# Performance work log

Hardware: AMD Instinct MI355X
Metric: run time of the kernel (lower is better)

## Reference

```python
import jax, jax.numpy as jnp
import numpy as np

H = 8        # heads
DH = 64      # dim_head
K = 16       # num_neighbors
EMB = 512    # emb_dim
INNER = H * DH
AINNER = 4 * DH  # per-head attn_mlp hidden width
POSH = 64


def setup_inputs() -> dict:
    key = jax.random.key(0)
    ks = jax.random.split(key, 20)
    bs, n = 2, 1024
    rn = lambda k, s, sc=1.0: jax.random.normal(k, s, jnp.float32) * sc
    return {
        "query": rn(ks[0], (bs, n, EMB)),
        "key_in": rn(ks[1], (bs, n, EMB)),
        "value": rn(ks[2], (bs, n, EMB)),
        "canonical": rn(ks[3], (bs, n, 3)),
        "w_q": rn(ks[4], (EMB, INNER), EMB ** -0.5),
        "w_k": rn(ks[5], (EMB, INNER), EMB ** -0.5),
        "w_v": rn(ks[6], (EMB, INNER), EMB ** -0.5),
        "w_out": rn(ks[7], (INNER, EMB), INNER ** -0.5),
        "b_out": rn(ks[8], (EMB,), 0.02),
        "pos_w1": rn(ks[9], (3, POSH), 3 ** -0.5),
        "pos_b1": rn(ks[10], (POSH,), 0.02),
        "pos_w2": rn(ks[11], (POSH, INNER), POSH ** -0.5),
        "pos_b2": rn(ks[12], (INNER,), 0.02),
        "aw1": rn(ks[13], (H, AINNER, DH), DH ** -0.5),   # grouped conv1 weight per head: (out=4*DH, in=DH)
        "ab1": rn(ks[14], (H, AINNER), 0.02),
        "aw2": rn(ks[15], (H, DH, AINNER), AINNER ** -0.5),  # grouped conv2: (out=DH, in=4*DH)
        "ab2": rn(ks[16], (H, DH), 0.02),
    }


def reference(query, key_in, value, canonical, w_q, w_k, w_v, w_out, b_out,
              pos_w1, pos_b1, pos_w2, pos_b2, aw1, ab1, aw2, ab2):
    bs, n, _ = query.shape
    # projections, then b n (h d) -> b h n d
    to_heads = lambda t: t.reshape(bs, n, H, DH).transpose(0, 2, 1, 3)
    q = to_heads(query @ w_q)
    k = to_heads(key_in @ w_k)
    v = to_heads(value @ w_v)

    # KNN on canonical coords: (b,n,n) squared distances, k smallest (includes self)
    d2 = jnp.sum((canonical[:, :, None, :] - canonical[:, None, :, :]) ** 2, axis=-1)
    _, nbr = jax.lax.top_k(-d2, K)                       # (b,n,K)
    idx = (nbr + (jnp.arange(bs) * n)[:, None, None]).reshape(-1)  # flat rows into bs*n

    # relative position embedding
    pos_nn = canonical.reshape(bs * n, 3)[idx].reshape(bs, n, K, 3)
    rel = pos_nn - canonical[:, :, None, :]
    rpe = jax.nn.relu(rel @ pos_w1 + pos_b1) @ pos_w2 + pos_b2        # (b,n,K,inner)
    rpe = rpe.reshape(bs, n, K, H, DH).transpose(0, 3, 1, 2, 4)       # (b,h,i,j,d)

    # faithful replication of the original view(bs*n,-1)[idx] gathers on (b,h,n,d) tensors
    gather = lambda t: t.reshape(bs * n, -1)[idx].reshape(bs, H, n, K, DH)
    qg, kg, vg = gather(q), gather(k), gather(v)
    vg = vg + rpe
    x = (qg - kg) + rpe                                  # (b,h,i,j,d)

    # grouped 1x1 conv attn_mlp == per-head MLP over d
    hdn = jax.nn.relu(jnp.einsum('bhijd,hed->bhije', x, aw1) + ab1[None, :, None, None, :])
    sim = jnp.einsum('bhije,hde->bhijd', hdn, aw2) + ab2[None, :, None, None, :]

    attn = jax.nn.softmax(sim, axis=3)                   # softmax over neighbors j
    norm = jnp.sqrt(jnp.sum(attn * attn, axis=2, keepdims=True))  # F.normalize over i
    attn = attn / jnp.maximum(norm, 1e-12)

    agg = jnp.einsum('bhijd,bhijd->bhid', attn, vg)      # (b,h,i,d)
    agg = agg.transpose(0, 2, 1, 3).reshape(bs, n, INNER)
    return agg @ w_out + b_out
```

## Files before the change

### kernel.cpp

```cpp
#include <hip/hip_runtime.h>


#define BS 2
#define NPT 1024
#define HH 8
#define DH 64
#define KNN 16
#define EMB 512
#define INNER 512
#define AINNER 256
#define POSH 64

typedef unsigned short u16;
typedef unsigned int u32;
typedef __attribute__((ext_vector_type(8))) short bf16x8;
typedef __attribute__((ext_vector_type(4))) float f32x4;

__device__ __forceinline__ float bf2f(u16 b) { union { u32 u; float f; } v; v.u = ((u32)b) << 16; return v.f; }
__device__ __forceinline__ u16 f2bf_rne(float f) {
    u32 x = __float_as_uint(f);
    u32 r = x + 0x7fffu + ((x >> 16) & 1u);
    return (u16)(r >> 16);
}
__device__ __forceinline__ void split2(float f, u16& hi, u16& lo) {
    u32 bits = __float_as_uint(f);
    hi = (u16)(bits >> 16);
    float resid = f - __uint_as_float(bits & 0xffff0000u);
    lo = (u16)(__float_as_uint(resid) >> 16);
}
__device__ __forceinline__ void split4(float4 f, ushort4& h, ushort4& l) {
    split2(f.x, h.x, l.x); split2(f.y, h.y, l.y);
    split2(f.z, h.z, l.z); split2(f.w, h.w, l.w);
}

__global__ __launch_bounds__(256) void k_pre(const float* __restrict__ aw1,
                                             const float* __restrict__ aw2,
                                             const float* __restrict__ pw2,
                                             u16* __restrict__ w1hi, u16* __restrict__ w2hi,
                                             u16* __restrict__ rw2hi)
{
    int idx = blockIdx.x * 256 + threadIdx.x;
    if (idx < 131072) {
        w1hi[idx] = f2bf_rne(aw1[idx]);
    } else if (idx < 262144) {
        int k2 = idx - 131072;
        w2hi[k2] = f2bf_rne(aw2[k2]);
    } else {
        int k2 = idx - 262144;
        int p = k2 & 63; int hd = k2 >> 6;
        int h = hd >> 6; int d = hd & 63;
        rw2hi[k2] = f2bf_rne(pw2[(size_t)p * INNER + h * DH + d]);
    }
}

__global__ __launch_bounds__(256) void k_split_T(const float* __restrict__ wq,
                                                 const float* __restrict__ wk,
                                                 const float* __restrict__ wv,
                                                 const float* __restrict__ wout,
                                                 u16* __restrict__ o0h, u16* __restrict__ o0l,
                                                 u16* __restrict__ o1h, u16* __restrict__ o1l,
                                                 u16* __restrict__ o2h, u16* __restrict__ o2l,
                                                 u16* __restrict__ o3h, u16* __restrict__ o3l)
{
    __shared__ float S[64][65];
    const int t = threadIdx.x;
    const int e0 = blockIdx.x * 64, c0 = blockIdx.y * 64;
    const float* src; u16* dh; u16* dl;
    switch (blockIdx.z) {
        case 0:  src = wq;   dh = o0h; dl = o0l; break;
        case 1:  src = wk;   dh = o1h; dl = o1l; break;
        case 2:  src = wv;   dh = o2h; dl = o2l; break;
        default: src = wout; dh = o3h; dl = o3l; break;
    }
    #pragma unroll
    for (int s = 0; s < 16; ++s) {
        int v = s * 256 + t; int r = v >> 6, c = v & 63;
        S[r][c] = src[(size_t)(e0 + r) * 512 + c0 + c];
    }
    __syncthreads();
    #pragma unroll
    for (int s = 0; s < 16; ++s) {
        int v = s * 256 + t; int c = v >> 6, e = v & 63;
        u16 hi, lo; split2(S[e][c], hi, lo);
        size_t off = (size_t)(c0 + c) * 512 + e0 + e;
        dh[off] = hi; dl[off] = lo;
    }
}

__global__ __launch_bounds__(256) void k_projM(const float* __restrict__ qf,
                                               const float* __restrict__ kf,
                                               const float* __restrict__ vf,
                                               const u16* __restrict__ wqh, const u16* __restrict__ wql,
                                               const u16* __restrict__ wkh, const u16* __restrict__ wkl,
                                               const u16* __restrict__ wvh, const u16* __restrict__ wvl,
                                               float* __restrict__ Dws, float* __restrict__ Vws)
{
    __shared__ u16 S[12][64 * 40];
    const int t = threadIdx.x, l = t & 63, w = t >> 6;
    const int lm = l & 15, lg = (l >> 4) * 8;
    const int g0 = blockIdx.x * 64, c0 = blockIdx.y * 64;
    const int sr = t >> 2, sc = (t & 3) * 8;

    f32x4 accD[4] = {{0,0,0,0},{0,0,0,0},{0,0,0,0},{0,0,0,0}};
    f32x4 accV[4] = {{0,0,0,0},{0,0,0,0},{0,0,0,0},{0,0,0,0}};

    const float* asrc0 = qf; const float* asrc1 = kf; const float* asrc2 = vf;

    for (int ks = 0; ks < 16; ++ks) {
        const int k0 = ks * 32;
        if (ks) __syncthreads();
        #pragma unroll
        for (int m = 0; m < 3; ++m) {
            const float* sp = (m == 0 ? asrc0 : (m == 1 ? asrc1 : asrc2))
                              + (size_t)(g0 + sr) * 512 + k0 + sc;
            float4 f0 = *(const float4*)sp;
            float4 f1 = *(const float4*)(sp + 4);
            if (m == 1) {
                f0.x = -f0.x; f0.y = -f0.y; f0.z = -f0.z; f0.w = -f0.w;
                f1.x = -f1.x; f1.y = -f1.y; f1.z = -f1.z; f1.w = -f1.w;
            }
            ushort4 h0, l0, h1, l1;
            split4(f0, h0, l0); split4(f1, h1, l1);
            *(ushort4*)&S[2*m  ][sr * 40 + sc]     = h0;
            *(ushort4*)&S[2*m  ][sr * 40 + sc + 4] = h1;
            *(ushort4*)&S[2*m+1][sr * 40 + sc]     = l0;
            *(ushort4*)&S[2*m+1][sr * 40 + sc + 4] = l1;
        }
        #define STG(p, base) \
            *(uint4*)&S[p][sr * 40 + sc] = *(const uint4*)&(base)[(size_t)(c0 + sr) * 512 + k0 + sc];
        STG(6, wqh) STG(7, wql) STG(8, wkh) STG(9, wkl) STG(10, wvh) STG(11, wvl)
        #undef STG
        __syncthreads();

        const int ao = (w * 16 + lm) * 40 + lg;
        bf16x8 aqh = *(const bf16x8*)&S[0][ao];
        bf16x8 aql = *(const bf16x8*)&S[1][ao];
        bf16x8 akh = *(const bf16x8*)&S[2][ao];
        bf16x8 akl = *(const bf16x8*)&S[3][ao];
        bf16x8 avh = *(const bf16x8*)&S[4][ao];
        bf16x8 avl = *(const bf16x8*)&S[5][ao];
        #pragma unroll
        for (int ct = 0; ct < 4; ++ct) {
            const int bo = (ct * 16 + lm) * 40 + lg;
            bf16x8 bqh = *(const bf16x8*)&S[6][bo];
            bf16x8 bql = *(const bf16x8*)&S[7][bo];
            bf16x8 bkh = *(const bf16x8*)&S[8][bo];
            bf16x8 bkl = *(const bf16x8*)&S[9][bo];
            bf16x8 bvh = *(const bf16x8*)&S[10][bo];
            bf16x8 bvl = *(const bf16x8*)&S[11][bo];
            accD[ct] = __builtin_amdgcn_mfma_f32_16x16x32_bf16(aqh, bqh, accD[ct], 0, 0, 0);
            accD[ct] = __builtin_amdgcn_mfma_f32_16x16x32_bf16(aql, bqh, accD[ct], 0, 0, 0);
            accD[ct] = __builtin_amdgcn_mfma_f32_16x16x32_bf16(aqh, bql, accD[ct], 0, 0, 0);
            accD[ct] = __builtin_amdgcn_mfma_f32_16x16x32_bf16(akh, bkh, accD[ct], 0, 0, 0);
            accD[ct] = __builtin_amdgcn_mfma_f32_16x16x32_bf16(akl, bkh, accD[ct], 0, 0, 0);
            accD[ct] = __builtin_amdgcn_mfma_f32_16x16x32_bf16(akh, bkl, accD[ct], 0, 0, 0);
            accV[ct] = __builtin_amdgcn_mfma_f32_16x16x32_bf16(avh, bvh, accV[ct], 0, 0, 0);
            accV[ct] = __builtin_amdgcn_mfma_f32_16x16x32_bf16(avl, bvh, accV[ct], 0, 0, 0);
            accV[ct] = __builtin_amdgcn_mfma_f32_16x16x32_bf16(avh, bvl, accV[ct], 0, 0, 0);
        }
    }

    const int b = blockIdx.x >> 4;
    const int h = blockIdx.y;
    #pragma unroll
    for (int ct = 0; ct < 4; ++ct) {
        #pragma unroll
        for (int r = 0; r < 4; ++r) {
            int g = g0 + w * 16 + (l >> 4) * 4 + r;
            int i = g & 1023;
            size_t off = (((size_t)(b * HH + h)) * NPT + i) * DH + ct * 16 + lm;
            Dws[off] = accD[ct][r];
            Vws[off] = accV[ct][r];
        }
    }
}

__global__ __launch_bounds__(256) void k_knn(const float* __restrict__ canonical, int* __restrict__ nbr)
{
    const int t = threadIdx.x, l = t & 63, w = t >> 6;
    const int i = blockIdx.x * 4 + w;
    const int b = blockIdx.y;
    const float* cb = canonical + (size_t)b * NPT * 3;
    const float qx = cb[i*3+0], qy = cb[i*3+1], qz = cb[i*3+2];
    float d2v[16];
    #pragma unroll
    for (int k = 0; k < 16; ++k) {
        int j = l * 16 + k;
        float dx = __fsub_rn(cb[j*3+0], qx);
        float dy = __fsub_rn(cb[j*3+1], qy);
        float dz = __fsub_rn(cb[j*3+2], qz);
        d2v[k] = __fadd_rn(__fadd_rn(__fmul_rn(dx,dx), __fmul_rn(dy,dy)), __fmul_rn(dz,dz));
    }
    unsigned alive = 0xFFFFu;
    int* out = nbr + ((size_t)b * NPT + i) * KNN;
    for (int sel = 0; sel < KNN; ++sel) {
        float bv = __builtin_inff(); int bk = 16;
        #pragma unroll
        for (int k = 0; k < 16; ++k) {
            float v = ((alive >> k) & 1u) ? d2v[k] : __builtin_inff();
            if (v < bv) { bv = v; bk = k; }
        }
        int bj = l * 16 + bk;
        #pragma unroll
        for (int m = 32; m >= 1; m >>= 1) {
            float ov = __shfl_xor(bv, m, 64);
            int   oj = __shfl_xor(bj, m, 64);
            if (ov < bv || (ov == bv && oj < bj)) { bv = ov; bj = oj; }
        }
        if (l == 0) out[sel] = bj;
        if ((bj >> 4) == l) alive &= ~(1u << (bj & 15));
    }
}

__global__ __launch_bounds__(256, 3) void k_attn(const float* __restrict__ Dws,
                                              const float* __restrict__ Vws,
                                              const float* __restrict__ canonical,
                                              const int* __restrict__ nbr,
                                              const float* __restrict__ pw1,
                                              const float* __restrict__ pb1,
                                              const float* __restrict__ pb2,
                                              const float* __restrict__ ab1,
                                              const float* __restrict__ ab2,
                                              const u16* __restrict__ w1hi,
                                              const u16* __restrict__ w2hi,
                                              const u16* __restrict__ rw2hi,
                                              u16* __restrict__ vvb,
                                              u16* __restrict__ attnb,
                                              float* __restrict__ npart2)
{
    const int it = blockIdx.x, h = blockIdx.y, b = blockIdx.z, t = threadIdx.x;
    const int l = t & 63, w = t >> 6;
    const int lm = l & 15, lg = (l >> 4) * 8;
    const int dd = w * 16 + lm;

    __shared__ u16 h1s[2][16 * 72];
    __shared__ u16 Xs[2][16 * 72];
    __shared__ u16 Hs[2][16 * 264];
    __shared__ u16 rw2s[64 * 72];
    __shared__ float pw1s[3 * POSH];
    __shared__ float pb1s[POSH];
    __shared__ float rel_all[8][KNN][3];
    __shared__ int nbrrow[KNN];

    bf16x8 w1f[8], w2f[8];
    float b1v[4];
    #pragma unroll
    for (int q = 0; q < 4; ++q) {
        int e = (w * 4 + q) * 16 + lm;
        b1v[q] = ab1[h * AINNER + e];
        #pragma unroll
        for (int kc = 0; kc < 2; ++kc)
            w1f[q*2+kc] = *(const bf16x8*)&w1hi[((size_t)(h * AINNER + e)) * DH + kc * 32 + lg];
    }
    const float b2v  = ab2[h * DH + dd];
    const float pb2v = pb2[h * DH + dd];
    #pragma unroll
    for (int kc = 0; kc < 8; ++kc)
        w2f[kc] = *(const bf16x8*)&w2hi[((size_t)(h * DH + dd)) * AINNER + kc * 32 + lg];

    for (int v = t; v < 64 * 64; v += 256) {
        int d = v >> 6, p = v & 63;
        rw2s[d * 72 + p] = rw2hi[(h * DH + d) * POSH + p];
    }
    if (t < 192) pw1s[t] = pw1[t];
    if (t < 64)  pb1s[t] = pb1[t];
    if (t < KNN) nbrrow[t] = nbr[((size_t)b * NPT + h * 128 + it) * KNN + t];
    if (t < 128) {
        int ti = t >> 4, jj = t & 15;
        int i2 = it * 8 + ti;
        int nv2 = nbr[((size_t)b * NPT + i2) * KNN + jj];
        const float* cn = canonical + ((size_t)b * NPT + nv2) * 3;
        const float* ci = canonical + ((size_t)b * NPT + i2) * 3;
        rel_all[ti][jj][0] = cn[0] - ci[0];
        rel_all[ti][jj][1] = cn[1] - ci[1];
        rel_all[ti][jj][2] = cn[2] - ci[2];
    }
    __syncthreads();

    float dvp[2][4], vwp[2][4];
    auto gather = [&](int pp) {
        #pragma unroll
        for (int u = 0; u < 2; ++u) {
            const int ti = 2 * pp + u;
            #pragma unroll
            for (int r = 0; r < 4; ++r) {
                int j = (l >> 4) * 4 + r;
                int nv = nbrrow[2 * ti + (j >> 3)];
                size_t off = (((size_t)b * HH + (nv >> 7)) * NPT + (nv & 127) * 8 + (j & 7)) * DH + dd;
                dvp[u][r] = Dws[off];
                vwp[u][r] = Vws[off];
            }
        }
    };
    gather(0);

    float npacc[4] = {0.f, 0.f, 0.f, 0.f};

    for (int p = 0; p < 4; ++p) {
        #pragma unroll
        for (int u = 0; u < 2; ++u) {
            const int ti = 2 * p + u;
            #pragma unroll
            for (int r = 0; r < 4; ++r) {
                int v = r * 256 + t; int j = v >> 6; int pp = v & 63;
                float a = pb1s[pp];
                a = fmaf(rel_all[ti][j][0], pw1s[pp], a);
                a = fmaf(rel_all[ti][j][1], pw1s[64 + pp], a);
                a = fmaf(rel_all[ti][j][2], pw1s[128 + pp], a);
                h1s[u][j * 72 + pp] = f2bf_rne(fmaxf(a, 0.0f));
            }
        }
        __syncthreads();
        #pragma unroll
        for (int u = 0; u < 2; ++u) {
            const int i = it * 8 + 2 * p + u;
            f32x4 racc = {0.f, 0.f, 0.f, 0.f};
            #pragma unroll
            for (int kc = 0; kc < 2; ++kc) {
                bf16x8 ah = *(const bf16x8*)&h1s[u][lm * 72 + kc * 32 + lg];
                bf16x8 rb = *(const bf16x8*)&rw2s[dd * 72 + kc * 32 + lg];
                racc = __builtin_amdgcn_mfma_f32_16x16x32_bf16(ah, rb, racc, 0, 0, 0);
            }
            u16* vvrow = vvb + (((size_t)(b * HH + h) * NPT + i) * KNN) * DH + dd;
            #pragma unroll
            for (int r = 0; r < 4; ++r) {
                int j = (l >> 4) * 4 + r;
                float rp = racc[r] + pb2v;
                Xs[u][j * 72 + dd] = f2bf_rne(dvp[u][r] + rp);
                vvrow[j * DH] = f2bf_rne(vwp[u][r] + rp);
            }
        }
        if (p < 3) gather(p + 1);
        __syncthreads();
        #pragma unroll
        for (int u = 0; u < 2; ++u) {
            f32x4 acc1[4] = {{0,0,0,0},{0,0,0,0},{0,0,0,0},{0,0,0,0}};
            #pragma unroll
            for (int kc = 0; kc < 2; ++kc) {
                bf16x8 ah = *(const bf16x8*)&Xs[u][lm * 72 + kc * 32 + lg];
                #pragma unroll
                for (int q = 0; q < 4; ++q)
                    acc1[q] = __builtin_amdgcn_mfma_f32_16x16x32_bf16(ah, w1f[q*2+kc], acc1[q], 0, 0, 0);
            }
            #pragma unroll
            for (int q = 0; q < 4; ++q) {
                int ee = (w * 4 + q) * 16 + lm;
                #pragma unroll
                for (int r = 0; r < 4; ++r) {
                    int jj = (l >> 4) * 4 + r;
                    Hs[u][jj * 264 + ee] = f2bf_rne(fmaxf(acc1[q][r] + b1v[q], 0.0f));
                }
            }
        }
        __syncthreads();
        #pragma unroll
        for (int u = 0; u < 2; ++u) {
            const int i = it * 8 + 2 * p + u;
            f32x4 acc2[4] = {{0,0,0,0},{0,0,0,0},{0,0,0,0},{0,0,0,0}};
            #pragma unroll
            for (int kc = 0; kc < 8; ++kc) {
                bf16x8 ah = *(const bf16x8*)&Hs[u][lm * 264 + kc * 32 + lg];
                acc2[kc & 3] = __builtin_amdgcn_mfma_f32_16x16x32_bf16(ah, w2f[kc], acc2[kc & 3], 0, 0, 0);
            }
            float sim[4];
            #pragma unroll
            for (int r = 0; r < 4; ++r)
                sim[r] = ((acc2[0][r] + acc2[1][r]) + (acc2[2][r] + acc2[3][r])) + b2v;
            float m = fmaxf(fmaxf(sim[0], sim[1]), fmaxf(sim[2], sim[3]));
            m = fmaxf(m, __shfl_xor(m, 16, 64));
            m = fmaxf(m, __shfl_xor(m, 32, 64));
            float ex[4], s = 0.0f;
            #pragma unroll
            for (int r = 0; r < 4; ++r) { ex[r] = __expf(sim[r] - m); s += ex[r]; }
            s += __shfl_xor(s, 16, 64);
            s += __shfl_xor(s, 32, 64);
            float inv = 1.0f / s;
            u16* ao = attnb + (((size_t)(b * HH + h) * NPT + i) * KNN) * DH + dd;
            #pragma unroll
            for (int r = 0; r < 4; ++r) {
                u16 abf16 = f2bf_rne(ex[r] * inv);
                ao[((l >> 4) * 4 + r) * DH] = abf16;
                float abf = bf2f(abf16);
                npacc[r] = fmaf(abf, abf, npacc[r]);
            }
        }
    }

    float* np = npart2 + ((size_t)((b * HH + h) * 128 + it)) * 1024 + ((l >> 4) * 4) * 64 + dd;
    #pragma unroll
    for (int r = 0; r < 4; ++r) np[r * 64] = npacc[r];
}

__global__ __launch_bounds__(256) void k_normR(const float* __restrict__ npart2, float* __restrict__ nrm)
{
    int v = blockIdx.x * 256 + threadIdx.x;
    int bh = v >> 10, jd = v & 1023;
    const float* src = npart2 + (size_t)bh * 128 * 1024 + jd;
    float s = 0.0f;
    for (int it2 = 0; it2 < 128; ++it2) s += src[(size_t)it2 * 1024];
    nrm[v] = sqrtf(s);
}

__global__ __launch_bounds__(256) void k_agg(const u16* __restrict__ attnb,
                                             const float* __restrict__ nrm,
                                             const u16* __restrict__ vvb,
                                             u16* __restrict__ agghi,
                                             u16* __restrict__ agglo)
{
    const int it = blockIdx.x, h = blockIdx.y, b = blockIdx.z, t = threadIdx.x;
    const int l = t & 63, w = t >> 6;
    const int i = it * 4 + w;
    __shared__ float rn[KNN * DH];
    for (int v = t; v < KNN * DH; v += 256)
        rn[v] = 1.0f / fmaxf(nrm[(size_t)(b * HH + h) * 1024 + v], 1e-12f);
    __syncthreads();
    const size_t row = ((size_t)(b * HH + h) * NPT + i) * (KNN * DH);
    bf16x8 a0 = *(const bf16x8*)&attnb[row + l * 8];
    bf16x8 a1 = *(const bf16x8*)&attnb[row + 512 + l * 8];
    bf16x8 q0 = *(const bf16x8*)&vvb[row + l * 8];
    bf16x8 q1 = *(const bf16x8*)&vvb[row + 512 + l * 8];
    const int dbase = (l & 7) * 8;
    float4 ra = *(const float4*)&rn[(l >> 3) * 64 + dbase];
    float4 rb = *(const float4*)&rn[(l >> 3) * 64 + dbase + 4];
    float4 rc = *(const float4*)&rn[(8 + (l >> 3)) * 64 + dbase];
    float4 rd = *(const float4*)&rn[(8 + (l >> 3)) * 64 + dbase + 4];
    const float r0[8] = {ra.x, ra.y, ra.z, ra.w, rb.x, rb.y, rb.z, rb.w};
    const float r1[8] = {rc.x, rc.y, rc.z, rc.w, rd.x, rd.y, rd.z, rd.w};
    float acc[8];
    #pragma unroll
    for (int e = 0; e < 8; ++e)
        acc[e] = bf2f((u16)a0[e]) * r0[e] * bf2f((u16)q0[e])
               + bf2f((u16)a1[e]) * r1[e] * bf2f((u16)q1[e]);
    #pragma unroll
    for (int mask = 8; mask <= 32; mask <<= 1)
        #pragma unroll
        for (int e = 0; e < 8; ++e)
            acc[e] += __shfl_xor(acc[e], mask, 64);
    if (l < 8) {
        size_t off = ((size_t)b * NPT + i) * INNER + h * DH + l * 8;
        ushort4 h0, l0, h1, l1;
        split2(acc[0], h0.x, l0.x); split2(acc[1], h0.y, l0.y);
        split2(acc[2], h0.z, l0.z); split2(acc[3], h0.w, l0.w);
        split2(acc[4], h1.x, l1.x); split2(acc[5], h1.y, l1.y);
        split2(acc[6], h1.z, l1.z); split2(acc[7], h1.w, l1.w);
        *(ushort4*)&agghi[off]     = h0;
        *(ushort4*)&agghi[off + 4] = h1;
        *(ushort4*)&agglo[off]     = l0;
        *(ushort4*)&agglo[off + 4] = l1;
    }
}

__global__ __launch_bounds__(256) void k_outM(const u16* __restrict__ agghi, const u16* __restrict__ agglo,
                                              const u16* __restrict__ wth, const u16* __restrict__ wtl,
                                              const float* __restrict__ bout,
                                              float* __restrict__ outp)
{
    __shared__ u16 S[4][64 * 40];
    const int t = threadIdx.x, l = t & 63, w = t >> 6;
    const int lm = l & 15, lg = (l >> 4) * 8;
    const int g0 = blockIdx.x * 64, c0 = blockIdx.y * 64;
    const int sr = t >> 2, sc = (t & 3) * 8;

    f32x4 acc[4] = {{0,0,0,0},{0,0,0,0},{0,0,0,0},{0,0,0,0}};
    float bv4[4];
    #pragma unroll
    for (int ct = 0; ct < 4; ++ct) bv4[ct] = bout[c0 + ct * 16 + lm];

    for (int ks = 0; ks < 16; ++ks) {
        const int k0 = ks * 32;
        if (ks) __syncthreads();
        *(uint4*)&S[0][sr * 40 + sc] = *(const uint4*)&agghi[(size_t)(g0 + sr) * 512 + k0 + sc];
        *(uint4*)&S[1][sr * 40 + sc] = *(const uint4*)&agglo[(size_t)(g0 + sr) * 512 + k0 + sc];
        *(uint4*)&S[2][sr * 40 + sc] = *(const uint4*)&wth[(size_t)(c0 + sr) * 512 + k0 + sc];
        *(uint4*)&S[3][sr * 40 + sc] = *(const uint4*)&wtl[(size_t)(c0 + sr) * 512 + k0 + sc];
        __syncthreads();

        const int ao = (w * 16 + lm) * 40 + lg;
        bf16x8 ah = *(const bf16x8*)&S[0][ao];
        bf16x8 al = *(const bf16x8*)&S[1][ao];
        #pragma unroll
        for (int ct = 0; ct < 4; ++ct) {
            const int bo = (ct * 16 + lm) * 40 + lg;
            bf16x8 bh = *(const bf16x8*)&S[2][bo];
            bf16x8 bl = *(const bf16x8*)&S[3][bo];
            acc[ct] = __builtin_amdgcn_mfma_f32_16x16x32_bf16(ah, bh, acc[ct], 0, 0, 0);
            acc[ct] = __builtin_amdgcn_mfma_f32_16x16x32_bf16(al, bh, acc[ct], 0, 0, 0);
            acc[ct] = __builtin_amdgcn_mfma_f32_16x16x32_bf16(ah, bl, acc[ct], 0, 0, 0);
        }
    }
    #pragma unroll
    for (int ct = 0; ct < 4; ++ct) {
        #pragma unroll
        for (int r = 0; r < 4; ++r) {
            int g = g0 + w * 16 + (l >> 4) * 4 + r;
            outp[(size_t)g * 512 + c0 + ct * 16 + lm] = acc[ct][r] + bv4[ct];
        }
    }
}

extern "C" void kernel_launch(void* const* d_in, const int* in_sizes, int n_in,
                              void* d_out, int out_size, void* d_ws, size_t ws_size,
                              hipStream_t stream) {
    const float* query     = (const float*)d_in[0];
    const float* key_in    = (const float*)d_in[1];
    const float* value     = (const float*)d_in[2];
    const float* canonical = (const float*)d_in[3];
    const float* wq   = (const float*)d_in[4];
    const float* wk   = (const float*)d_in[5];
    const float* wv   = (const float*)d_in[6];
    const float* wout = (const float*)d_in[7];
    const float* bout = (const float*)d_in[8];
    const float* pw1  = (const float*)d_in[9];
    const float* pb1  = (const float*)d_in[10];
    const float* pw2  = (const float*)d_in[11];
    const float* pb2  = (const float*)d_in[12];
    const float* aw1  = (const float*)d_in[13];
    const float* ab1  = (const float*)d_in[14];
    const float* aw2  = (const float*)d_in[15];
    const float* ab2  = (const float*)d_in[16];

    float* ws    = (float*)d_ws;
    float* Dws   = ws;
    float* Vws   = ws + 1048576;
    float* aggp  = ws + 2097152;
    float* nrm   = ws + 3162112;
    int*   nbr   = (int*)(ws + 3293184);
    float* attnR = ws + 3325952;

    u16* agghi = (u16*)aggp;
    u16* agglo = agghi + 1048576;

    u16* attnb = (u16*)attnR;
    u16* pl   = (u16*)(attnR + 8388608);
    u16* wqTh = pl;                u16* wqTl = pl + 262144;
    u16* wkTh = pl + 524288;       u16* wkTl = pl + 786432;
    u16* wvTh = pl + 1048576;      u16* wvTl = pl + 1310720;
    float* npart2 = attnR + 12582912;

    u16* u16b  = (u16*)(ws + 20103168);
    u16* w1hi  = u16b;
    u16* w2hi  = u16b + 262144;
    u16* rw2hi = u16b + 524288;
    u16* vvb   = u16b + 589824;
    u16* wouTh = u16b + 17367040;
    u16* wouTl = u16b + 17629184;

    k_pre<<<1152, 256, 0, stream>>>(aw1, aw2, pw2, w1hi, w2hi, rw2hi);
    k_split_T<<<dim3(8, 8, 4), 256, 0, stream>>>(wq, wk, wv, wout,
                                                 wqTh, wqTl, wkTh, wkTl, wvTh, wvTl, wouTh, wouTl);
    k_projM<<<dim3(32, 8), 256, 0, stream>>>(query, key_in, value,
                                             wqTh, wqTl, wkTh, wkTl, wvTh, wvTl, Dws, Vws);
    k_knn<<<dim3(256, BS), 256, 0, stream>>>(canonical, nbr);
    k_attn<<<dim3(128, HH, BS), 256, 0, stream>>>(Dws, Vws, canonical, nbr, pw1, pb1, pb2,
                                                  ab1, ab2, w1hi, w2hi, rw2hi, vvb, attnb, npart2);
    k_normR<<<64, 256, 0, stream>>>(npart2, nrm);
    k_agg<<<dim3(256, HH, BS), 256, 0, stream>>>(attnb, nrm, vvb, agghi, agglo);
    k_outM<<<dim3(32, 8), 256, 0, stream>>>(agghi, agglo, wouTh, wouTl, bout, (float*)d_out);
}
```

Baseline: 152.4 us.

## Merge weight prep kernels, move pos-MLP layer 1 into KNN, split norm reduction

Merges the two weight-conversion kernels into one launch. The first positional-MLP layer (relu(rel@pw1+pb1)) now runs in the KNN kernel and is written to global memory as bf16. The attention kernel then loads it directly as MFMA operands, which drops per-head recomputation, shared staging and one barrier per iteration. The norm reduction is split across four waves per output to get more parallelism. The trade-off is an extra global buffer of hidden activations that must be written once and read by every head.

```diff
diff --git a/kernel.cpp b/kernel.cpp
--- a/kernel.cpp
+++ b/kernel.cpp
@@ -33,40 +33,41 @@
     split2(f.z, h.z, l.z); split2(f.w, h.w, l.w);
 }
 
-__global__ __launch_bounds__(256) void k_pre(const float* __restrict__ aw1,
-                                             const float* __restrict__ aw2,
-                                             const float* __restrict__ pw2,
-                                             u16* __restrict__ w1hi, u16* __restrict__ w2hi,
-                                             u16* __restrict__ rw2hi)
-{
-    int idx = blockIdx.x * 256 + threadIdx.x;
-    if (idx < 131072) {
-        w1hi[idx] = f2bf_rne(aw1[idx]);
-    } else if (idx < 262144) {
-        int k2 = idx - 131072;
-        w2hi[k2] = f2bf_rne(aw2[k2]);
-    } else {
-        int k2 = idx - 262144;
-        int p = k2 & 63; int hd = k2 >> 6;
-        int h = hd >> 6; int d = hd & 63;
-        rw2hi[k2] = f2bf_rne(pw2[(size_t)p * INNER + h * DH + d]);
-    }
-}
-
-__global__ __launch_bounds__(256) void k_split_T(const float* __restrict__ wq,
-                                                 const float* __restrict__ wk,
-                                                 const float* __restrict__ wv,
-                                                 const float* __restrict__ wout,
-                                                 u16* __restrict__ o0h, u16* __restrict__ o0l,
-                                                 u16* __restrict__ o1h, u16* __restrict__ o1l,
-                                                 u16* __restrict__ o2h, u16* __restrict__ o2l,
-                                                 u16* __restrict__ o3h, u16* __restrict__ o3l)
+__global__ __launch_bounds__(256) void k_preT(const float* __restrict__ aw1,
+                                              const float* __restrict__ aw2,
+                                              const float* __restrict__ pw2,
+                                              const float* __restrict__ wq,
+                                              const float* __restrict__ wk,
+                                              const float* __restrict__ wv,
+                                              const float* __restrict__ wout,
+                                              u16* __restrict__ w1hi, u16* __restrict__ w2hi,
+                                              u16* __restrict__ rw2hi,
+                                              u16* __restrict__ o0h, u16* __restrict__ o0l,
+                                              u16* __restrict__ o1h, u16* __restrict__ o1l,
+                                              u16* __restrict__ o2h, u16* __restrict__ o2l,
+                                              u16* __restrict__ o3h, u16* __restrict__ o3l)
 {
     __shared__ float S[64][65];
-    const int t = threadIdx.x;
-    const int e0 = blockIdx.x * 64, c0 = blockIdx.y * 64;
+    const int bx = blockIdx.x, t = threadIdx.x;
+    if (bx < 1152) {
+        int idx = bx * 256 + t;
+        if (idx < 131072) {
+            w1hi[idx] = f2bf_rne(aw1[idx]);
+        } else if (idx < 262144) {
+            int k2 = idx - 131072;
+            w2hi[k2] = f2bf_rne(aw2[k2]);
+        } else {
+            int k2 = idx - 262144;
+            int p = k2 & 63; int hd = k2 >> 6;
+            int h = hd >> 6; int d = hd & 63;
+            rw2hi[k2] = f2bf_rne(pw2[(size_t)p * INNER + h * DH + d]);
+        }
+        return;
+    }
+    const int v0 = bx - 1152;
+    const int e0 = (v0 & 7) * 64, c0 = ((v0 >> 3) & 7) * 64, z = v0 >> 6;
     const float* src; u16* dh; u16* dl;
-    switch (blockIdx.z) {
+    switch (z) {
         case 0:  src = wq;   dh = o0h; dl = o0l; break;
         case 1:  src = wk;   dh = o1h; dl = o1l; break;
         case 2:  src = wv;   dh = o2h; dl = o2l; break;
@@ -104,14 +105,12 @@
     f32x4 accD[4] = {{0,0,0,0},{0,0,0,0},{0,0,0,0},{0,0,0,0}};
     f32x4 accV[4] = {{0,0,0,0},{0,0,0,0},{0,0,0,0},{0,0,0,0}};
 
-    const float* asrc0 = qf; const float* asrc1 = kf; const float* asrc2 = vf;
-
     for (int ks = 0; ks < 16; ++ks) {
         const int k0 = ks * 32;
         if (ks) __syncthreads();
         #pragma unroll
         for (int m = 0; m < 3; ++m) {
-            const float* sp = (m == 0 ? asrc0 : (m == 1 ? asrc1 : asrc2))
+            const float* sp = (m == 0 ? qf : (m == 1 ? kf : vf))
                               + (size_t)(g0 + sr) * 512 + k0 + sc;
             float4 f0 = *(const float4*)sp;
             float4 f1 = *(const float4*)(sp + 4);
@@ -175,7 +174,11 @@
     }
 }
 
-__global__ __launch_bounds__(256) void k_knn(const float* __restrict__ canonical, int* __restrict__ nbr)
+__global__ __launch_bounds__(256) void k_knn(const float* __restrict__ canonical,
+                                             const float* __restrict__ pw1,
+                                             const float* __restrict__ pb1,
+                                             int* __restrict__ nbr,
+                                             u16* __restrict__ h1g)
 {
     const int t = threadIdx.x, l = t & 63, w = t >> 6;
     const int i = blockIdx.x * 4 + w;
@@ -192,7 +195,9 @@
         d2v[k] = __fadd_rn(__fadd_rn(__fmul_rn(dx,dx), __fmul_rn(dy,dy)), __fmul_rn(dz,dz));
     }
     unsigned alive = 0xFFFFu;
+    int js[16];
     int* out = nbr + ((size_t)b * NPT + i) * KNN;
+    #pragma unroll
     for (int sel = 0; sel < KNN; ++sel) {
         float bv = __builtin_inff(); int bk = 16;
         #pragma unroll
@@ -208,22 +213,35 @@
             if (ov < bv || (ov == bv && oj < bj)) { bv = ov; bj = oj; }
         }
         if (l == 0) out[sel] = bj;
+        js[sel] = bj;
         if ((bj >> 4) == l) alive &= ~(1u << (bj & 15));
+    }
+    const float pw10 = pw1[l], pw11 = pw1[64 + l], pw12 = pw1[128 + l], pb1v = pb1[l];
+    u16* hrow = h1g + (((size_t)b * NPT + i) * KNN) * 64 + l;
+    #pragma unroll
+    for (int j = 0; j < KNN; ++j) {
+        int nv = js[j];
+        float rx = cb[nv*3+0] - qx;
+        float ry = cb[nv*3+1] - qy;
+        float rz = cb[nv*3+2] - qz;
+        float a = pb1v;
+        a = fmaf(rx, pw10, a);
+        a = fmaf(ry, pw11, a);
+        a = fmaf(rz, pw12, a);
+        hrow[j * 64] = f2bf_rne(fmaxf(a, 0.0f));
     }
 }
 
 __global__ __launch_bounds__(256, 3) void k_attn(const float* __restrict__ Dws,
                                               const float* __restrict__ Vws,
-                                              const float* __restrict__ canonical,
                                               const int* __restrict__ nbr,
-                                              const float* __restrict__ pw1,
-                                              const float* __restrict__ pb1,
                                               const float* __restrict__ pb2,
                                               const float* __restrict__ ab1,
                                               const float* __restrict__ ab2,
                                               const u16* __restrict__ w1hi,
                                               const u16* __restrict__ w2hi,
                                               const u16* __restrict__ rw2hi,
+                                              const u16* __restrict__ h1g,
                                               u16* __restrict__ vvb,
                                               u16* __restrict__ attnb,
                                               float* __restrict__ npart2)
@@ -233,13 +251,9 @@
     const int lm = l & 15, lg = (l >> 4) * 8;
     const int dd = w * 16 + lm;
 
-    __shared__ u16 h1s[2][16 * 72];
     __shared__ u16 Xs[2][16 * 72];
     __shared__ u16 Hs[2][16 * 264];
     __shared__ u16 rw2s[64 * 72];
-    __shared__ float pw1s[3 * POSH];
-    __shared__ float pb1s[POSH];
-    __shared__ float rel_all[8][KNN][3];
     __shared__ int nbrrow[KNN];
 
     bf16x8 w1f[8], w2f[8];
@@ -262,26 +276,16 @@
         int d = v >> 6, p = v & 63;
         rw2s[d * 72 + p] = rw2hi[(h * DH + d) * POSH + p];
     }
-    if (t < 192) pw1s[t] = pw1[t];
-    if (t < 64)  pb1s[t] = pb1[t];
     if (t < KNN) nbrrow[t] = nbr[((size_t)b * NPT + h * 128 + it) * KNN + t];
-    if (t < 128) {
-        int ti = t >> 4, jj = t & 15;
-        int i2 = it * 8 + ti;
-        int nv2 = nbr[((size_t)b * NPT + i2) * KNN + jj];
-        const float* cn = canonical + ((size_t)b * NPT + nv2) * 3;
-        const float* ci = canonical + ((size_t)b * NPT + i2) * 3;
-        rel_all[ti][jj][0] = cn[0] - ci[0];
-        rel_all[ti][jj][1] = cn[1] - ci[1];
-        rel_all[ti][jj][2] = cn[2] - ci[2];
-    }
     __syncthreads();
 
     float dvp[2][4], vwp[2][4];
+    bf16x8 h1f[2][2];
     auto gather = [&](int pp) {
         #pragma unroll
         for (int u = 0; u < 2; ++u) {
             const int ti = 2 * pp + u;
+            const int i = it * 8 + ti;
             #pragma unroll
             for (int r = 0; r < 4; ++r) {
                 int j = (l >> 4) * 4 + r;
@@ -290,6 +294,9 @@
                 dvp[u][r] = Dws[off];
                 vwp[u][r] = Vws[off];
             }
+            const u16* hb = h1g + (((size_t)b * NPT + i) * KNN + lm) * 64;
+            h1f[u][0] = *(const bf16x8*)&hb[lg];
+            h1f[u][1] = *(const bf16x8*)&hb[32 + lg];
         }
     };
     gather(0);
@@ -297,29 +304,14 @@
     float npacc[4] = {0.f, 0.f, 0.f, 0.f};
 
     for (int p = 0; p < 4; ++p) {
-        #pragma unroll
-        for (int u = 0; u < 2; ++u) {
-            const int ti = 2 * p + u;
-            #pragma unroll
-            for (int r = 0; r < 4; ++r) {
-                int v = r * 256 + t; int j = v >> 6; int pp = v & 63;
-                float a = pb1s[pp];
-                a = fmaf(rel_all[ti][j][0], pw1s[pp], a);
-                a = fmaf(rel_all[ti][j][1], pw1s[64 + pp], a);
-                a = fmaf(rel_all[ti][j][2], pw1s[128 + pp], a);
-                h1s[u][j * 72 + pp] = f2bf_rne(fmaxf(a, 0.0f));
-            }
-        }
-        __syncthreads();
         #pragma unroll
         for (int u = 0; u < 2; ++u) {
             const int i = it * 8 + 2 * p + u;
             f32x4 racc = {0.f, 0.f, 0.f, 0.f};
             #pragma unroll
             for (int kc = 0; kc < 2; ++kc) {
-                bf16x8 ah = *(const bf16x8*)&h1s[u][lm * 72 + kc * 32 + lg];
                 bf16x8 rb = *(const bf16x8*)&rw2s[dd * 72 + kc * 32 + lg];
-                racc = __builtin_amdgcn_mfma_f32_16x16x32_bf16(ah, rb, racc, 0, 0, 0);
+                racc = __builtin_amdgcn_mfma_f32_16x16x32_bf16(h1f[u][kc], rb, racc, 0, 0, 0);
             }
             u16* vvrow = vvb + (((size_t)(b * HH + h) * NPT + i) * KNN) * DH + dd;
             #pragma unroll
@@ -393,12 +385,21 @@
 
 __global__ __launch_bounds__(256) void k_normR(const float* __restrict__ npart2, float* __restrict__ nrm)
 {
-    int v = blockIdx.x * 256 + threadIdx.x;
-    int bh = v >> 10, jd = v & 1023;
-    const float* src = npart2 + (size_t)bh * 128 * 1024 + jd;
+    __shared__ float red[256];
+    const int vout = blockIdx.x * 64 + (threadIdx.x & 63);
+    const int chunk = threadIdx.x >> 6;
+    const int bh = vout >> 10, jd = vout & 1023;
+    const float* src = npart2 + (size_t)bh * 131072 + jd + (size_t)chunk * 32768;
     float s = 0.0f;
-    for (int it2 = 0; it2 < 128; ++it2) s += src[(size_t)it2 * 1024];
-    nrm[v] = sqrtf(s);
+    #pragma unroll 4
+    for (int k = 0; k < 32; ++k) s += src[k * 1024];
+    red[threadIdx.x] = s;
+    __syncthreads();
+    if (chunk == 0) {
+        float tot = (red[threadIdx.x] + red[threadIdx.x + 64])
+                  + (red[threadIdx.x + 128] + red[threadIdx.x + 192]);
+        nrm[vout] = sqrtf(tot);
+    }
 }
 
 __global__ __launch_bounds__(256) void k_agg(const u16* __restrict__ attnb,
@@ -536,6 +537,7 @@
     u16* wkTh = pl + 524288;       u16* wkTl = pl + 786432;
     u16* wvTh = pl + 1048576;      u16* wvTl = pl + 1310720;
     float* npart2 = attnR + 12582912;
+    u16* h1g = (u16*)(attnR + 14680064);
 
     u16* u16b  = (u16*)(ws + 20103168);
     u16* w1hi  = u16b;
@@ -545,15 +547,15 @@
     u16* wouTh = u16b + 17367040;
     u16* wouTl = u16b + 17629184;
 
-    k_pre<<<1152, 256, 0, stream>>>(aw1, aw2, pw2, w1hi, w2hi, rw2hi);
-    k_split_T<<<dim3(8, 8, 4), 256, 0, stream>>>(wq, wk, wv, wout,
-                                                 wqTh, wqTl, wkTh, wkTl, wvTh, wvTl, wouTh, wouTl);
+    k_preT<<<1408, 256, 0, stream>>>(aw1, aw2, pw2, wq, wk, wv, wout,
+                                     w1hi, w2hi, rw2hi,
+                                     wqTh, wqTl, wkTh, wkTl, wvTh, wvTl, wouTh, wouTl);
+    k_knn<<<dim3(256, BS), 256, 0, stream>>>(canonical, pw1, pb1, nbr, h1g);
     k_projM<<<dim3(32, 8), 256, 0, stream>>>(query, key_in, value,
                                              wqTh, wqTl, wkTh, wkTl, wvTh, wvTl, Dws, Vws);
-    k_knn<<<dim3(256, BS), 256, 0, stream>>>(canonical, nbr);
-    k_attn<<<dim3(128, HH, BS), 256, 0, stream>>>(Dws, Vws, canonical, nbr, pw1, pb1, pb2,
-                                                  ab1, ab2, w1hi, w2hi, rw2hi, vvb, attnb, npart2);
-    k_normR<<<64, 256, 0, stream>>>(npart2, nrm);
+    k_attn<<<dim3(128, HH, BS), 256, 0, stream>>>(Dws, Vws, nbr, pb2, ab1, ab2,
+                                                  w1hi, w2hi, rw2hi, h1g, vvb, attnb, npart2);
+    k_normR<<<256, 256, 0, stream>>>(npart2, nrm);
     k_agg<<<dim3(256, HH, BS), 256, 0, stream>>>(attnb, nrm, vvb, agghi, agglo);
     k_outM<<<dim3(32, 8), 256, 0, stream>>>(agghi, agglo, wouTh, wouTl, bout, (float*)d_out);
 }
```

New measurement: 148.4 us. 1.03x faster.
